# Performance work log

Measured on AMD Instinct MI355X. Metric: run time of the kernel, lower is better.

Reference implementation:

```python
import jax, jax.numpy as jnp
import numpy as np
from jax.ops import segment_sum

IN_DIM, HID_DIM, OUT_DIM = 128, 128, 64
N_NODES, N_EDGES = 50000, 800000


def gcn_conv(x, src, dst, W, b, n_nodes):
    # Symmetric GCN normalization (no self loops): deg at targets from unit weights
    deg = segment_sum(jnp.ones(src.shape[0], dtype=x.dtype), dst, num_segments=n_nodes)
    dinv = jnp.where(deg > 0, jax.lax.rsqrt(jnp.maximum(deg, 1.0)), 0.0)
    norm = dinv[src] * dinv[dst]                      # [E]
    h = x @ W                                         # [N, out] small GEMM first (PyG order)
    msg = h[src] * norm[:, None]                      # gather + scale: [E, out]
    out = segment_sum(msg, dst, num_segments=n_nodes) # scatter-add to targets
    return out + b


def setup_inputs() -> dict:
    key = jax.random.key(0)
    k1, k2, k3, k4, k5 = jax.random.split(key, 5)
    x = jax.random.normal(k1, (N_NODES, IN_DIM), dtype=jnp.float32)
    edge_index = jax.random.randint(k2, (2, N_EDGES), 0, N_NODES, dtype=jnp.int64)
    s1 = 1.0 / np.sqrt(IN_DIM)
    s2 = 1.0 / np.sqrt(HID_DIM)
    W1 = jax.random.uniform(k3, (IN_DIM, HID_DIM), jnp.float32, -s1, s1)
    b1 = jnp.zeros((HID_DIM,), jnp.float32)
    W2 = jax.random.uniform(k4, (HID_DIM, OUT_DIM), jnp.float32, -s2, s2)
    b2 = jnp.zeros((OUT_DIM,), jnp.float32)
    return {"x": x, "edge_index": edge_index, "W1": W1, "b1": b1, "W2": W2, "b2": b2}


def reference(x, edge_index, W1, b1, W2, b2):
    n_nodes = x.shape[0]
    src, dst = edge_index[0], edge_index[1]
    h = gcn_conv(x, src, dst, W1, b1, n_nodes)
    h = jax.nn.relu(h)
    # Dropout is identity in eval mode (reference is deterministic)
    out = gcn_conv(h, src, dst, W2, b2, n_nodes)
    return out
```

## Files before the change

### kernel.cpp

```cpp
#include <hip/hip_runtime.h>

#define N_NODES 50000
#define N_EDGES 800000
#define IN_DIM  128
#define HID_DIM 128
#define OUT_DIM 64

#define NPAD 50176
#define CAP  64
#define GEMM1B ((N_NODES + 63) / 64)
#define FILLB (N_EDGES / 256)
#define INITB 24

typedef __attribute__((ext_vector_type(8))) short bf16x8;
typedef __attribute__((ext_vector_type(4))) float f32x4;

__device__ __forceinline__ unsigned short f2bf(float f) {
    unsigned u = __float_as_uint(f);
    u += 0x7fffu + ((u >> 16) & 1u);
    return (unsigned short)(u >> 16);
}
__device__ __forceinline__ float bflo(unsigned u) { return __uint_as_float(u << 16); }
__device__ __forceinline__ float bfhi(unsigned u) { return __uint_as_float(u & 0xffff0000u); }

#define ACC8(u)  do { \
    acc[0] += bflo(u.x); acc[1] += bfhi(u.x); \
    acc[2] += bflo(u.y); acc[3] += bfhi(u.y); \
    acc[4] += bflo(u.z); acc[5] += bfhi(u.z); \
    acc[6] += bflo(u.w); acc[7] += bfhi(u.w); } while (0)

#define FMA8(u, sc_)  do { \
    acc[0] += bflo(u.x) * (sc_); acc[1] += bfhi(u.x) * (sc_); \
    acc[2] += bflo(u.y) * (sc_); acc[3] += bfhi(u.y) * (sc_); \
    acc[4] += bflo(u.z) * (sc_); acc[5] += bfhi(u.z) * (sc_); \
    acc[6] += bflo(u.w) * (sc_); acc[7] += bfhi(u.w) * (sc_); } while (0)

__device__ __forceinline__ float deg2dinv(int deg) {
    return (deg > 0) ? rsqrtf((float)deg) : 0.0f;
}


__global__ __launch_bounds__(256) void init_kernel(const float* __restrict__ W1,
                                                   const float* __restrict__ W2,
                                                   unsigned short* __restrict__ w1t,
                                                   unsigned short* __restrict__ w2t,
                                                   int* __restrict__ cnt) {
    int bid = blockIdx.x;
    int tid = threadIdx.x;
    if (bid < 16) {
        int idx = bid * 256 + tid;
        int c = idx >> 5, k4 = (idx & 31) * 4;
        ushort4 o;
        o.x = f2bf(W1[(k4 + 0) * 128 + c]);
        o.y = f2bf(W1[(k4 + 1) * 128 + c]);
        o.z = f2bf(W1[(k4 + 2) * 128 + c]);
        o.w = f2bf(W1[(k4 + 3) * 128 + c]);
        *(ushort4*)(w1t + c * 128 + k4) = o;
    } else {
        int idx = (bid - 16) * 256 + tid;
        int c = idx >> 5, k4 = (idx & 31) * 4;
        ushort4 o;
        o.x = f2bf(W2[(k4 + 0) * 64 + c]);
        o.y = f2bf(W2[(k4 + 1) * 64 + c]);
        o.z = f2bf(W2[(k4 + 2) * 64 + c]);
        o.w = f2bf(W2[(k4 + 3) * 64 + c]);
        *(ushort4*)(w2t + c * 128 + k4) = o;
    }
    int4 z = {0, 0, 0, 0};
    for (int i = bid * 256 + tid; i < NPAD / 4; i += INITB * 256)
        ((int4*)cnt)[i] = z;
}


__global__ __launch_bounds__(256) void fill_gemm1_kernel(const int* __restrict__ src,
                                                         const int* __restrict__ dst,
                                                         int* __restrict__ cnt,
                                                         unsigned short* __restrict__ csr_src,
                                                         const float* __restrict__ x,
                                                         const unsigned short* __restrict__ w1t,
                                                         unsigned short* __restrict__ h1b) {
    int bid = blockIdx.x;
    if (bid < FILLB) {
        int e = bid * 256 + threadIdx.x;
        int s = src[e], d = dst[e];
        int slot = atomicAdd(&cnt[d], 1);
        if (slot < CAP) csr_src[(d << 6) + slot] = (unsigned short)s;
        return;
    }

    int gb = bid - FILLB;
    int wave = threadIdx.x >> 6;
    int lane = threadIdx.x & 63;
    int n = lane & 15, quad = lane >> 4;
    int row0 = gb * 64 + wave * 16;

    int arow = row0 + n;
    if (arow >= N_NODES) arow = N_NODES - 1;
    const float* aptr = x + (size_t)arow * 128 + quad * 8;
    const unsigned short* bbase = w1t + (size_t)n * 128 + quad * 8;

    f32x4 acc[8];
#pragma unroll
    for (int t = 0; t < 8; ++t) acc[t] = (f32x4){0.f, 0.f, 0.f, 0.f};

#pragma unroll
    for (int w4 = 0; w4 < 4; ++w4) {
        float4 f0 = *(const float4*)(aptr + w4 * 32);
        float4 f1 = *(const float4*)(aptr + w4 * 32 + 4);
        bf16x8 af;
        af[0] = (short)f2bf(f0.x); af[1] = (short)f2bf(f0.y);
        af[2] = (short)f2bf(f0.z); af[3] = (short)f2bf(f0.w);
        af[4] = (short)f2bf(f1.x); af[5] = (short)f2bf(f1.y);
        af[6] = (short)f2bf(f1.z); af[7] = (short)f2bf(f1.w);
#pragma unroll
        for (int t = 0; t < 8; ++t) {
            bf16x8 bf = *(const bf16x8*)(bbase + (size_t)t * 2048 + w4 * 32);
            acc[t] = __builtin_amdgcn_mfma_f32_16x16x32_bf16(af, bf, acc[t], 0, 0, 0);
        }
    }

#pragma unroll
    for (int r = 0; r < 4; ++r) {
        int row = row0 + quad * 4 + r;
        if (row < N_NODES) {
            unsigned short* o = h1b + (size_t)row * 128 + n;
#pragma unroll
            for (int t = 0; t < 8; ++t) o[t * 16] = f2bf(acc[t][r]);
        }
    }
}


#define A1T_STRIDE 136

__global__ __launch_bounds__(256) void agg1_gemm2_fused(const unsigned short* __restrict__ csr_src,
                                                        const int* __restrict__ cnt,
                                                        const float* __restrict__ b1,
                                                        const unsigned short* __restrict__ h1b,
                                                        const unsigned short* __restrict__ w2t,
                                                        unsigned short* __restrict__ h2b) {
    __shared__ unsigned short a1t[16 * A1T_STRIDE];

    int node0 = blockIdx.x * 16;
    int g = threadIdx.x >> 4;
    int q = threadIdx.x & 15;
    int node = node0 + g;
    int start = node << 6;
    int m = cnt[node];
    float dn = deg2dinv(m);
    if (m > CAP) m = CAP;

    float acc[8] = {};
    int j = 0;
    for (; j + 7 < m; j += 8) {
        ushort4 sa = *(const ushort4*)(csr_src + start + j);
        ushort4 sb = *(const ushort4*)(csr_src + start + j + 4);
        float d0 = deg2dinv(cnt[sa.x]);
        float d1 = deg2dinv(cnt[sa.y]);
        float d2 = deg2dinv(cnt[sa.z]);
        float d3 = deg2dinv(cnt[sa.w]);
        float d4 = deg2dinv(cnt[sb.x]);
        float d5 = deg2dinv(cnt[sb.y]);
        float d6 = deg2dinv(cnt[sb.z]);
        float d7 = deg2dinv(cnt[sb.w]);
        uint4 u0 = ((const uint4*)(h1b + (size_t)sa.x * 128))[q];
        uint4 u1 = ((const uint4*)(h1b + (size_t)sa.y * 128))[q];
        uint4 u2 = ((const uint4*)(h1b + (size_t)sa.z * 128))[q];
        uint4 u3 = ((const uint4*)(h1b + (size_t)sa.w * 128))[q];
        uint4 u4 = ((const uint4*)(h1b + (size_t)sb.x * 128))[q];
        uint4 u5 = ((const uint4*)(h1b + (size_t)sb.y * 128))[q];
        uint4 u6 = ((const uint4*)(h1b + (size_t)sb.z * 128))[q];
        uint4 u7 = ((const uint4*)(h1b + (size_t)sb.w * 128))[q];
        FMA8(u0, d0); FMA8(u1, d1); FMA8(u2, d2); FMA8(u3, d3);
        FMA8(u4, d4); FMA8(u5, d5); FMA8(u6, d6); FMA8(u7, d7);
    }
    for (; j + 3 < m; j += 4) {
        ushort4 sa = *(const ushort4*)(csr_src + start + j);
        float d0 = deg2dinv(cnt[sa.x]);
        float d1 = deg2dinv(cnt[sa.y]);
        float d2 = deg2dinv(cnt[sa.z]);
        float d3 = deg2dinv(cnt[sa.w]);
        uint4 u0 = ((const uint4*)(h1b + (size_t)sa.x * 128))[q];
        uint4 u1 = ((const uint4*)(h1b + (size_t)sa.y * 128))[q];
        uint4 u2 = ((const uint4*)(h1b + (size_t)sa.z * 128))[q];
        uint4 u3 = ((const uint4*)(h1b + (size_t)sa.w * 128))[q];
        FMA8(u0, d0); FMA8(u1, d1); FMA8(u2, d2); FMA8(u3, d3);
    }
    for (; j < m; ++j) {
        int s0 = csr_src[start + j];
        float d0 = deg2dinv(cnt[s0]);
        uint4 u0 = ((const uint4*)(h1b + (size_t)s0 * 128))[q];
        FMA8(u0, d0);
    }

    {
        float4 bA = ((const float4*)b1)[2 * q];
        float4 bB = ((const float4*)b1)[2 * q + 1];
        ushort4 oA, oB;
        oA.x = f2bf(fmaxf(acc[0] * dn + bA.x, 0.f));
        oA.y = f2bf(fmaxf(acc[1] * dn + bA.y, 0.f));
        oA.z = f2bf(fmaxf(acc[2] * dn + bA.z, 0.f));
        oA.w = f2bf(fmaxf(acc[3] * dn + bA.w, 0.f));
        oB.x = f2bf(fmaxf(acc[4] * dn + bB.x, 0.f));
        oB.y = f2bf(fmaxf(acc[5] * dn + bB.y, 0.f));
        oB.z = f2bf(fmaxf(acc[6] * dn + bB.z, 0.f));
        oB.w = f2bf(fmaxf(acc[7] * dn + bB.w, 0.f));
        ushort4* o = (ushort4*)(a1t + g * A1T_STRIDE + q * 8);
        o[0] = oA;
        o[1] = oB;
    }
    __syncthreads();

    int wave = threadIdx.x >> 6;
    int lane = threadIdx.x & 63;
    int n = lane & 15, quad = lane >> 4;
    const unsigned short* bbase = w2t + (size_t)(wave * 16 + n) * 128 + quad * 8;
    const unsigned short* abase = a1t + (size_t)n * A1T_STRIDE + quad * 8;

    f32x4 c2 = (f32x4){0.f, 0.f, 0.f, 0.f};
#pragma unroll
    for (int w4 = 0; w4 < 4; ++w4) {
        bf16x8 af = *(const bf16x8*)(abase + w4 * 32);
        bf16x8 bf = *(const bf16x8*)(bbase + w4 * 32);
        c2 = __builtin_amdgcn_mfma_f32_16x16x32_bf16(af, bf, c2, 0, 0, 0);
    }

#pragma unroll
    for (int r = 0; r < 4; ++r) {
        int row = node0 + quad * 4 + r;
        float dr = deg2dinv(cnt[row]);
        h2b[(size_t)row * 64 + wave * 16 + n] = f2bf(c2[r] * dr);
    }
}


__global__ __launch_bounds__(256) void agg2_kernel(const unsigned short* __restrict__ csr_src,
                                                   const int* __restrict__ cnt,
                                                   const float* __restrict__ b2,
                                                   const unsigned short* __restrict__ h2b,
                                                   float* __restrict__ out) {
    int node = blockIdx.x * 4 + (threadIdx.x >> 6);
    if (node >= N_NODES) return;
    int lane = threadIdx.x & 63;
    int grp = lane >> 3;
    int q   = lane & 7;
    int start = node << 6;
    int m = cnt[node];
    float dn = deg2dinv(m);
    if (m > CAP) m = CAP;

    float acc[8] = {};

    int j = grp;
    for (; j + 8 < m; j += 16) {
        int s0 = csr_src[start + j];
        int s1 = csr_src[start + j + 8];
        uint4 u0 = ((const uint4*)(h2b + (size_t)s0 * 64))[q];
        uint4 u1 = ((const uint4*)(h2b + (size_t)s1 * 64))[q];
        ACC8(u0); ACC8(u1);
    }
    if (j < m) {
        int s0 = csr_src[start + j];
        uint4 u0 = ((const uint4*)(h2b + (size_t)s0 * 64))[q];
        ACC8(u0);
    }

#pragma unroll
    for (int d = 8; d <= 32; d <<= 1) {
#pragma unroll
        for (int c = 0; c < 8; ++c) acc[c] += __shfl_xor(acc[c], d, 64);
    }

    if (lane < 8) {
        float4 bA = ((const float4*)b2)[2 * q];
        float4 bB = ((const float4*)b2)[2 * q + 1];
        float4 rA, rB;
        rA.x = acc[0] * dn + bA.x;
        rA.y = acc[1] * dn + bA.y;
        rA.z = acc[2] * dn + bA.z;
        rA.w = acc[3] * dn + bA.w;
        rB.x = acc[4] * dn + bB.x;
        rB.y = acc[5] * dn + bB.y;
        rB.z = acc[6] * dn + bB.z;
        rB.w = acc[7] * dn + bB.w;
        float4* o = (float4*)(out + (size_t)node * 64);
        o[2 * q] = rA;
        o[2 * q + 1] = rB;
    }
}


extern "C" void kernel_launch(void* const* d_in, const int* in_sizes, int n_in,
                              void* d_out, int out_size, void* d_ws, size_t ws_size,
                              hipStream_t stream) {
    const float* x  = (const float*)d_in[0];
    const int*   ei = (const int*)d_in[1];
    const float* W1 = (const float*)d_in[2];
    const float* b1 = (const float*)d_in[3];
    const float* W2 = (const float*)d_in[4];
    const float* b2 = (const float*)d_in[5];
    float* out = (float*)d_out;

    const int* src = ei;
    const int* dst = ei + N_EDGES;

    char* ws = (char*)d_ws;
    int*   cnt       = (int*)ws;
    unsigned short* csr_src = (unsigned short*)(cnt + NPAD);
    unsigned short* h1b = csr_src + (size_t)N_NODES * CAP;
    unsigned short* h2b = h1b + (size_t)N_NODES * HID_DIM;
    unsigned short* w1t = h2b + (size_t)N_NODES * OUT_DIM;
    unsigned short* w2t = w1t + 128 * 128;

    init_kernel<<<INITB, 256, 0, stream>>>(W1, W2, w1t, w2t, cnt);

    fill_gemm1_kernel<<<FILLB + GEMM1B, 256, 0, stream>>>(src, dst, cnt, csr_src,
                                                          x, w1t, h1b);

    agg1_gemm2_fused<<<N_NODES / 16, 256, 0, stream>>>(csr_src, cnt, b1, h1b, w2t, h2b);

    agg2_kernel<<<(N_NODES + 3) / 4, 256, 0, stream>>>(csr_src, cnt, b2, h2b, out);
}
```

Baseline: 215.8 us.

## Fold W1 transpose into GEMM1 via shared memory and split fill into separate kernel

The standalone init kernel goes away. Each GEMM1 block now converts and transposes W1 into padded LDS itself and also zeroes part of the degree counters. The W2 transpose moves into the edge-fill kernel, which now runs after GEMM1 instead of being co-scheduled with it. The launch count stays at four, but every GEMM1 block repeats the W1 conversion, and the atomic fill no longer overlaps the GEMM.

```diff
diff --git a/kernel.cpp b/kernel.cpp
--- a/kernel.cpp
+++ b/kernel.cpp
@@ -10,7 +10,7 @@
 #define CAP  64
 #define GEMM1B ((N_NODES + 63) / 64)
 #define FILLB (N_EDGES / 256)
-#define INITB 24
+#define W2PREPB 8
 
 typedef __attribute__((ext_vector_type(8))) short bf16x8;
 typedef __attribute__((ext_vector_type(4))) float f32x4;
@@ -39,65 +39,39 @@
     return (deg > 0) ? rsqrtf((float)deg) : 0.0f;
 }
 
-
-__global__ __launch_bounds__(256) void init_kernel(const float* __restrict__ W1,
-                                                   const float* __restrict__ W2,
-                                                   unsigned short* __restrict__ w1t,
-                                                   unsigned short* __restrict__ w2t,
-                                                   int* __restrict__ cnt) {
-    int bid = blockIdx.x;
+#define W1T_STRIDE 136
+
+
+__global__ __launch_bounds__(256) void gemm1_kernel(const float* __restrict__ x,
+                                                    const float* __restrict__ W1,
+                                                    int* __restrict__ cnt,
+                                                    unsigned short* __restrict__ h1b) {
+    __shared__ unsigned short w1t[128 * W1T_STRIDE];
+
     int tid = threadIdx.x;
-    if (bid < 16) {
-        int idx = bid * 256 + tid;
-        int c = idx >> 5, k4 = (idx & 31) * 4;
-        ushort4 o;
-        o.x = f2bf(W1[(k4 + 0) * 128 + c]);
-        o.y = f2bf(W1[(k4 + 1) * 128 + c]);
-        o.z = f2bf(W1[(k4 + 2) * 128 + c]);
-        o.w = f2bf(W1[(k4 + 3) * 128 + c]);
-        *(ushort4*)(w1t + c * 128 + k4) = o;
-    } else {
-        int idx = (bid - 16) * 256 + tid;
-        int c = idx >> 5, k4 = (idx & 31) * 4;
-        ushort4 o;
-        o.x = f2bf(W2[(k4 + 0) * 64 + c]);
-        o.y = f2bf(W2[(k4 + 1) * 64 + c]);
-        o.z = f2bf(W2[(k4 + 2) * 64 + c]);
-        o.w = f2bf(W2[(k4 + 3) * 64 + c]);
-        *(ushort4*)(w2t + c * 128 + k4) = o;
-    }
-    int4 z = {0, 0, 0, 0};
-    for (int i = bid * 256 + tid; i < NPAD / 4; i += INITB * 256)
-        ((int4*)cnt)[i] = z;
-}
-
-
-__global__ __launch_bounds__(256) void fill_gemm1_kernel(const int* __restrict__ src,
-                                                         const int* __restrict__ dst,
-                                                         int* __restrict__ cnt,
-                                                         unsigned short* __restrict__ csr_src,
-                                                         const float* __restrict__ x,
-                                                         const unsigned short* __restrict__ w1t,
-                                                         unsigned short* __restrict__ h1b) {
-    int bid = blockIdx.x;
-    if (bid < FILLB) {
-        int e = bid * 256 + threadIdx.x;
-        int s = src[e], d = dst[e];
-        int slot = atomicAdd(&cnt[d], 1);
-        if (slot < CAP) csr_src[(d << 6) + slot] = (unsigned short)s;
-        return;
-    }
-
-    int gb = bid - FILLB;
-    int wave = threadIdx.x >> 6;
-    int lane = threadIdx.x & 63;
+    int zi = blockIdx.x * 256 + tid;
+    if (zi < NPAD / 4) {
+        int4 z = {0, 0, 0, 0};
+        ((int4*)cnt)[zi] = z;
+    }
+
+#pragma unroll
+    for (int i = 0; i < 64; ++i) {
+        int idx = i * 256 + tid;
+        int k = idx >> 7, c = idx & 127;
+        w1t[c * W1T_STRIDE + k] = f2bf(W1[idx]);
+    }
+    __syncthreads();
+
+    int wave = tid >> 6;
+    int lane = tid & 63;
     int n = lane & 15, quad = lane >> 4;
-    int row0 = gb * 64 + wave * 16;
+    int row0 = blockIdx.x * 64 + wave * 16;
 
     int arow = row0 + n;
     if (arow >= N_NODES) arow = N_NODES - 1;
     const float* aptr = x + (size_t)arow * 128 + quad * 8;
-    const unsigned short* bbase = w1t + (size_t)n * 128 + quad * 8;
+    const unsigned short* bbase = w1t + (size_t)n * W1T_STRIDE + quad * 8;
 
     f32x4 acc[8];
 #pragma unroll
@@ -114,7 +88,7 @@
         af[6] = (short)f2bf(f1.z); af[7] = (short)f2bf(f1.w);
 #pragma unroll
         for (int t = 0; t < 8; ++t) {
-            bf16x8 bf = *(const bf16x8*)(bbase + (size_t)t * 2048 + w4 * 32);
+            bf16x8 bf = *(const bf16x8*)(bbase + (size_t)t * 16 * W1T_STRIDE + w4 * 32);
             acc[t] = __builtin_amdgcn_mfma_f32_16x16x32_bf16(af, bf, acc[t], 0, 0, 0);
         }
     }
@@ -127,6 +101,32 @@
 #pragma unroll
             for (int t = 0; t < 8; ++t) o[t * 16] = f2bf(acc[t][r]);
         }
+    }
+}
+
+
+__global__ __launch_bounds__(256) void prep_fill_kernel(const int* __restrict__ src,
+                                                        const int* __restrict__ dst,
+                                                        int* __restrict__ cnt,
+                                                        unsigned short* __restrict__ csr_src,
+                                                        const float* __restrict__ W2,
+                                                        unsigned short* __restrict__ w2t) {
+    int bid = blockIdx.x;
+    int tid = threadIdx.x;
+    if (bid < W2PREPB) {
+        int idx = bid * 256 + tid;
+        int c = idx >> 5, k4 = (idx & 31) * 4;
+        ushort4 o;
+        o.x = f2bf(W2[(k4 + 0) * 64 + c]);
+        o.y = f2bf(W2[(k4 + 1) * 64 + c]);
+        o.z = f2bf(W2[(k4 + 2) * 64 + c]);
+        o.w = f2bf(W2[(k4 + 3) * 64 + c]);
+        *(ushort4*)(w2t + c * 128 + k4) = o;
+    } else {
+        int e = (bid - W2PREPB) * 256 + tid;
+        int s = src[e], d = dst[e];
+        int slot = atomicAdd(&cnt[d], 1);
+        if (slot < CAP) csr_src[(d << 6) + slot] = (unsigned short)s;
     }
 }
 
@@ -309,13 +309,12 @@
     unsigned short* csr_src = (unsigned short*)(cnt + NPAD);
     unsigned short* h1b = csr_src + (size_t)N_NODES * CAP;
     unsigned short* h2b = h1b + (size_t)N_NODES * HID_DIM;
-    unsigned short* w1t = h2b + (size_t)N_NODES * OUT_DIM;
-    unsigned short* w2t = w1t + 128 * 128;
-
-    init_kernel<<<INITB, 256, 0, stream>>>(W1, W2, w1t, w2t, cnt);
-
-    fill_gemm1_kernel<<<FILLB + GEMM1B, 256, 0, stream>>>(src, dst, cnt, csr_src,
-                                                          x, w1t, h1b);
+    unsigned short* w2t = h2b + (size_t)N_NODES * OUT_DIM;
+
+    gemm1_kernel<<<GEMM1B, 256, 0, stream>>>(x, W1, cnt, h1b);
+
+    prep_fill_kernel<<<W2PREPB + FILLB, 256, 0, stream>>>(src, dst, cnt, csr_src,
+                                                          W2, w2t);
 
     agg1_gemm2_fused<<<N_NODES / 16, 256, 0, stream>>>(csr_src, cnt, b1, h1b, w2t, h2b);
 
```

After: 197.6 us. -8.4%, faster.
